# Kernel tuning notes

Hardware: AMD Instinct MI355X
Metric: run time of the kernel (lower is better)

## Reference

```python
import jax, jax.numpy as jnp
import numpy as np

ROT_DELTA = 1  # rotation_delta from __init__
BN_EPS = 1e-3  # keras BatchNormalization default epsilon


def conv_dirac(signal, bc_idx, bc_w, W, b):
    """Template-based intrinsic mesh conv (dirac patch operator).

    signal: [N, D]; bc_idx/bc_w: [N, Rr, A, 3]; W: [T, Rr, A, D]; b: [T].
    Returns [N, K, T] with K = A // ROT_DELTA rotations.
    """
    gathered = signal[bc_idx]  # [N, Rr, A, 3, D] irregular gather
    interp = jnp.einsum('vrai,vraid->vrad', bc_w, gathered)  # barycentric interp
    A = interp.shape[2]
    rots = np.arange(0, A, ROT_DELTA)
    # Rotating the (small) template weights is equivalent to rolling the
    # interpolated signal along the angular axis, but far cheaper.
    W_rot = jnp.stack([jnp.roll(W, int(r), axis=2) for r in rots])  # [K, T, Rr, A, D]
    return jnp.einsum('vrad,ktrad->vkt', interp, W_rot) + b  # [N, K, T]


def angular_max_pool(x):
    # Select, per vertex, the rotation whose response has maximal L2 norm.
    k = jnp.argmax(jnp.linalg.norm(x, axis=-1), axis=1)  # [N]
    return jnp.take_along_axis(x, k[:, None, None], axis=1)[:, 0]  # [N, T]


def batch_norm(x, gamma, beta):
    mu = jnp.mean(x, axis=0, keepdims=True)
    var = jnp.var(x, axis=0, keepdims=True)
    return gamma * (x - mu) * jax.lax.rsqrt(var + BN_EPS) + beta


def setup_inputs() -> dict:
    key = jax.random.key(0)
    ks = jax.random.split(key, 6)
    N, Rr, A, D, T = 80000, 5, 8, 32, 32
    signal = jax.random.normal(ks[0], (N, D), dtype=jnp.float32)
    bc_idx = jax.random.randint(ks[1], (N, Rr, A, 3), 0, N)
    bc_w = jax.random.uniform(ks[2], (N, Rr, A, 3), dtype=jnp.float32)
    bc_w = bc_w / jnp.sum(bc_w, axis=-1, keepdims=True)  # barycentric coords sum to 1
    W1 = jax.random.normal(ks[3], (T, Rr, A, D), dtype=jnp.float32) * 0.05
    W2 = jax.random.normal(ks[4], (T, Rr, A, D), dtype=jnp.float32) * 0.05
    return {
        'signal': signal, 'bc_idx': bc_idx, 'bc_w': bc_w,
        'W1': W1, 'b1': jnp.zeros((T,), jnp.float32),
        'gamma1': jnp.ones((T,), jnp.float32), 'beta1': jnp.zeros((T,), jnp.float32),
        'W2': W2, 'b2': jnp.zeros((T,), jnp.float32),
        'gamma2': jnp.ones((T,), jnp.float32), 'beta2': jnp.zeros((T,), jnp.float32),
    }


def reference(signal, bc_idx, bc_w, W1, b1, gamma1, beta1, W2, b2, gamma2, beta2):
    # Branch 1: conv -> angular max-pool -> BN -> relu
    s = conv_dirac(signal, bc_idx, bc_w, W1, b1)
    s = angular_max_pool(s)
    s = batch_norm(s, gamma1, beta1)
    s = jax.nn.relu(s)
    # Branch 2: conv -> angular max-pool -> BN
    s = conv_dirac(s, bc_idx, bc_w, W2, b2)
    s = angular_max_pool(s)
    s = batch_norm(s, gamma2, beta2)
    # Residual add (input_dim == amt_templates -> no rescale branch) + activation
    return jax.nn.relu(s + signal)
```

## Files before the change

### kernel.cpp

```cpp
#include <hip/hip_runtime.h>
#include <math.h>

#define RR 5
#define AA 8
#define DD 32
#define TT 32
#define KK 8
#define MM 1280

#define RT2 0.70710678118654752f

typedef float v2f __attribute__((ext_vector_type(2)));
typedef float v4f __attribute__((ext_vector_type(4)));

static __device__ __forceinline__ v2f pkfma(v2f a, v2f b, v2f c) {
#if __has_builtin(__builtin_elementwise_fma)
    return __builtin_elementwise_fma(a, b, c);
#else
    v2f r; r.x = fmaf(a.x, b.x, c.x); r.y = fmaf(a.y, b.y, c.y); return r;
#endif
}

__global__ void wdft_kernel(const float* __restrict__ W, float* __restrict__ Ws) {
    int idx = blockIdx.x * 256 + threadIdx.x;
    if (idx >= TT * RR * DD) return;
    int d = idx & 31;
    int tr = idx >> 5;
    float xa[8];
    #pragma unroll
    for (int a = 0; a < 8; ++a) xa[a] = W[(tr * 8 + a) * 32 + d];
    float s0 = xa[0] + xa[4], d0 = xa[0] - xa[4];
    float s1 = xa[1] + xa[5], d1 = xa[1] - xa[5];
    float s2 = xa[2] + xa[6], d2 = xa[2] - xa[6];
    float s3 = xa[3] + xa[7], d3 = xa[3] - xa[7];
    float s02 = s0 + s2, s13 = s1 + s3;
    float F0 = s02 + s13, F4 = s02 - s13;
    float R2 = s0 - s2, I2 = s3 - s1;
    float u = RT2 * (d1 - d3), v = RT2 * (d1 + d3);
    float R1 = d0 + u, R3 = d0 - u;
    float I1 = -d2 - v, I3 = d2 - v;
    float* o = &Ws[tr * 256 + d * 8];
    o[0] = F0; o[1] = F4; o[2] = R1; o[3] = I1;
    o[4] = R2; o[5] = I2; o[6] = R3; o[7] = I3;
}

__global__ __launch_bounds__(256, 2)
void fused_conv_kernel(const float* __restrict__ sig,
                       const int* __restrict__ bc_idx,
                       const float* __restrict__ bc_w,
                       const float* __restrict__ Wsg,
                       const float* __restrict__ bias,
                       float* __restrict__ s_out,
                       int N) {
    __shared__ float Wl[32 * 260];
    __shared__ float Is[32 * 260];

    int tid = threadIdx.x;
    int vBase = blockIdx.x * 32;

    int lane = tid & 63;
    int wv = tid >> 6;
    int vi = lane & 7;
    int tg = lane >> 3;
    int vLocal = wv * 8 + vi;
    int v = vBase + vLocal;
    bool valid = v < N;

    int d2 = tid & 15;
    int g = tid >> 4;

    v2f A0[4], A1[4], A2[4], A3[4];
    #pragma unroll
    for (int j = 0; j < 4; ++j) {
        A0[j] = (v2f){0.f, 0.f}; A1[j] = (v2f){0.f, 0.f};
        A2[j] = (v2f){0.f, 0.f}; A3[j] = (v2f){0.f, 0.f};
    }

    const float4* Ws4 = (const float4*)Wsg;
    const v2f rt2 = {RT2, RT2};

    for (int r = 0; r < RR; ++r) {
        __syncthreads();

        for (int i2 = tid; i2 < 2048; i2 += 256) {
            int t = i2 >> 6;
            int u4 = i2 & 63;
            float4 val = Ws4[(t * 5 + r) * 64 + u4];
            *(float4*)&Wl[t * 260 + u4 * 4] = val;
        }

        #pragma unroll
        for (int vv0 = 0; vv0 < 2; ++vv0) {
            int vv = g + vv0 * 16;
            int vg = vBase + vv;
            int vgc = (vg < N) ? vg : (N - 1);
            int base = (vgc * 40 + r * 8) * 3;
            v2f xa[8];
            #pragma unroll
            for (int a = 0; a < 8; ++a) {
                int i0 = bc_idx[base + a * 3 + 0];
                int i1 = bc_idx[base + a * 3 + 1];
                int i2 = bc_idx[base + a * 3 + 2];
                float w0 = bc_w[base + a * 3 + 0];
                float w1 = bc_w[base + a * 3 + 1];
                float w2 = bc_w[base + a * 3 + 2];
                v2f r0 = *(const v2f*)&sig[(size_t)i0 * 32 + 2 * d2];
                v2f r1 = *(const v2f*)&sig[(size_t)i1 * 32 + 2 * d2];
                v2f r2 = *(const v2f*)&sig[(size_t)i2 * 32 + 2 * d2];
                v2f w0v = {w0, w0};
                v2f w1v = {w1, w1};
                v2f w2v = {w2, w2};
                xa[a] = pkfma(w2v, r2, pkfma(w1v, r1, w0v * r0));
            }
            v2f s0 = xa[0] + xa[4], dd0 = xa[0] - xa[4];
            v2f s1 = xa[1] + xa[5], dd1 = xa[1] - xa[5];
            v2f s2 = xa[2] + xa[6], dd2 = xa[2] - xa[6];
            v2f s3 = xa[3] + xa[7], dd3 = xa[3] - xa[7];
            v2f s02 = s0 + s2, s13 = s1 + s3;
            v2f F0 = s02 + s13, F4 = s02 - s13;
            v2f R2 = s0 - s2, I2 = s3 - s1;
            v2f u = rt2 * (dd1 - dd3), vv_ = rt2 * (dd1 + dd3);
            v2f R1 = dd0 + u, R3 = dd0 - u;
            v2f I1 = -dd2 - vv_, I3 = dd2 - vv_;
            float* ob = &Is[vv * 260 + (2 * d2) * 8];
            v4f lo0 = {F0.x, F4.x, R1.x, I1.x};
            v4f lo1 = {R2.x, I2.x, R3.x, I3.x};
            v4f hi0 = {F0.y, F4.y, R1.y, I1.y};
            v4f hi1 = {R2.y, I2.y, R3.y, I3.y};
            *(v4f*)&ob[0] = lo0;
            *(v4f*)&ob[4] = lo1;
            *(v4f*)&ob[8] = hi0;
            *(v4f*)&ob[12] = hi1;
        }
        __syncthreads();

        const float* ip = &Is[vLocal * 260];
        const float* wp = &Wl[tg * 260];
        #pragma unroll 4
        for (int d = 0; d < 32; ++d) {
            v4f p0 = *(const v4f*)&ip[d * 8];
            v4f p1 = *(const v4f*)&ip[d * 8 + 4];
            v2f x04 = p0.xy;
            v2f x1 = p0.zw;
            v2f x2 = p1.xy;
            v2f x3 = p1.zw;
            v2f x1n = {x1.y, -x1.x};
            v2f x2n = {x2.y, -x2.x};
            v2f x3n = {x3.y, -x3.x};
            #pragma unroll
            for (int j = 0; j < 4; ++j) {
                v4f q0 = *(const v4f*)&wp[j * 8 * 260 + d * 8];
                v4f q1 = *(const v4f*)&wp[j * 8 * 260 + d * 8 + 4];
                A0[j] = pkfma(x04, q0.xy, A0[j]);
                A1[j] = pkfma(x1, (v2f){q0.z, q0.z}, A1[j]);
                A1[j] = pkfma(x1n, (v2f){q0.w, q0.w}, A1[j]);
                A2[j] = pkfma(x2, (v2f){q1.x, q1.x}, A2[j]);
                A2[j] = pkfma(x2n, (v2f){q1.y, q1.y}, A2[j]);
                A3[j] = pkfma(x3, (v2f){q1.z, q1.z}, A3[j]);
                A3[j] = pkfma(x3n, (v2f){q1.w, q1.w}, A3[j]);
            }
        }
    }

    float outk[8][4];
    #pragma unroll
    for (int j = 0; j < 4; ++j) {
        float C0 = A0[j].x, C4 = A0[j].y;
        float R1 = A1[j].x, I1 = A1[j].y;
        float R2 = A2[j].x, I2 = A2[j].y;
        float R3 = A3[j].x, I3 = A3[j].y;
        float e = 0.125f * (C0 + C4), o = 0.125f * (C0 - C4);
        float p = 0.25f * (R1 + R3), q = 0.25f * R2, s = 0.25f * (I1 - I3);
        float a_ = 0.25f * RT2 * (R1 - R3);
        float b_ = 0.25f * RT2 * (I1 + I3);
        float c_ = 0.25f * I2;
        float bb = bias[tg + 8 * j];
        outk[0][j] = e + p + q + bb;
        outk[1][j] = o + a_ - b_ - c_ + bb;
        outk[2][j] = e - s - q + bb;
        outk[3][j] = o - a_ - b_ + c_ + bb;
        outk[4][j] = e - p + q + bb;
        outk[5][j] = o - a_ + b_ - c_ + bb;
        outk[6][j] = e + s - q + bb;
        outk[7][j] = o + a_ + b_ + c_ + bb;
    }

    float best = -1.f;
    int bk = 0;
    #pragma unroll
    for (int k = 0; k < 8; ++k) {
        float nl = outk[k][0] * outk[k][0] + outk[k][1] * outk[k][1]
                 + outk[k][2] * outk[k][2] + outk[k][3] * outk[k][3];
        nl += __shfl_xor(nl, 8);
        nl += __shfl_xor(nl, 16);
        nl += __shfl_xor(nl, 32);
        float n = sqrtf(nl);
        if (n > best) { best = n; bk = k; }
    }

    if (valid) {
        float sel0 = 0.f, sel1 = 0.f, sel2 = 0.f, sel3 = 0.f;
        #pragma unroll
        for (int k = 0; k < 8; ++k) {
            if (k == bk) { sel0 = outk[k][0]; sel1 = outk[k][1]; sel2 = outk[k][2]; sel3 = outk[k][3]; }
        }
        float* o = s_out + (size_t)v * 32 + tg;
        o[0]  = sel0;
        o[8]  = sel1;
        o[16] = sel2;
        o[24] = sel3;
    }
}

__global__ void stats_kernel(const float* __restrict__ s,
                             double* __restrict__ sums,
                             double* __restrict__ sumsq, int n) {
    __shared__ double la[256];
    __shared__ double lb[256];
    int tid = threadIdx.x;
    int t = tid & 31;
    int row = tid >> 5;
    double a = 0.0, b = 0.0;
    for (int v = blockIdx.x * 8 + row; v < n; v += gridDim.x * 8) {
        float x = s[(size_t)v * 32 + t];
        a += (double)x;
        b += (double)x * (double)x;
    }
    la[tid] = a; lb[tid] = b;
    __syncthreads();
    for (int off = 128; off >= 32; off >>= 1) {
        if (tid < off) { la[tid] += la[tid + off]; lb[tid] += lb[tid + off]; }
        __syncthreads();
    }
    if (tid < 32) {
        atomicAdd(&sums[t], la[tid]);
        atomicAdd(&sumsq[t], lb[tid]);
    }
}

__global__ void finalize_kernel(const double* __restrict__ sums,
                                const double* __restrict__ sumsq,
                                const float* __restrict__ gamma,
                                const float* __restrict__ beta,
                                float* __restrict__ scale,
                                float* __restrict__ shift, int n) {
    int t = threadIdx.x;
    if (t < 32) {
        double mu = sums[t] / (double)n;
        double var = sumsq[t] / (double)n - mu * mu;
        double sc = (double)gamma[t] / sqrt(var + 1e-3);
        scale[t] = (float)sc;
        shift[t] = (float)((double)beta[t] - mu * sc);
    }
}

__global__ void affine_relu_kernel(const float* __restrict__ s,
                                   const float* __restrict__ scale,
                                   const float* __restrict__ shift,
                                   float* __restrict__ o, int n4) {
    int e = blockIdx.x * blockDim.x + threadIdx.x;
    if (e >= n4) return;
    int t0 = (e & 7) * 4;
    float4 x = ((const float4*)s)[e];
    float4 y;
    y.x = fmaxf(fmaf(scale[t0 + 0], x.x, shift[t0 + 0]), 0.f);
    y.y = fmaxf(fmaf(scale[t0 + 1], x.y, shift[t0 + 1]), 0.f);
    y.z = fmaxf(fmaf(scale[t0 + 2], x.z, shift[t0 + 2]), 0.f);
    y.w = fmaxf(fmaf(scale[t0 + 3], x.w, shift[t0 + 3]), 0.f);
    ((float4*)o)[e] = y;
}

__global__ void final_kernel(const float* __restrict__ s,
                             const float* __restrict__ scale,
                             const float* __restrict__ shift,
                             const float* __restrict__ sig,
                             float* __restrict__ o, int n4) {
    int e = blockIdx.x * blockDim.x + threadIdx.x;
    if (e >= n4) return;
    int t0 = (e & 7) * 4;
    float4 x = ((const float4*)s)[e];
    float4 z = ((const float4*)sig)[e];
    float4 y;
    y.x = fmaxf(fmaf(scale[t0 + 0], x.x, shift[t0 + 0]) + z.x, 0.f);
    y.y = fmaxf(fmaf(scale[t0 + 1], x.y, shift[t0 + 1]) + z.y, 0.f);
    y.z = fmaxf(fmaf(scale[t0 + 2], x.z, shift[t0 + 2]) + z.z, 0.f);
    y.w = fmaxf(fmaf(scale[t0 + 3], x.w, shift[t0 + 3]) + z.w, 0.f);
    ((float4*)o)[e] = y;
}

__global__ void zero_stats_kernel(double* __restrict__ d, float* __restrict__ f) {
    int t = threadIdx.x;
    if (t < 128) d[t] = 0.0;
    if (t < 128) f[t] = 0.f;
}

extern "C" void kernel_launch(void* const* d_in, const int* in_sizes, int n_in,
                              void* d_out, int out_size, void* d_ws, size_t ws_size,
                              hipStream_t stream) {
    const float* signal = (const float*)d_in[0];
    const int* bc_idx   = (const int*)d_in[1];
    const float* bc_w   = (const float*)d_in[2];
    const float* W1     = (const float*)d_in[3];
    const float* b1     = (const float*)d_in[4];
    const float* g1     = (const float*)d_in[5];
    const float* be1    = (const float*)d_in[6];
    const float* W2     = (const float*)d_in[7];
    const float* b2     = (const float*)d_in[8];
    const float* g2     = (const float*)d_in[9];
    const float* be2    = (const float*)d_in[10];
    float* out = (float*)d_out;

    const int N = in_sizes[0] / 32;

    char* ws = (char*)d_ws;
    double* sums1  = (double*)ws;
    double* sumsq1 = sums1 + 32;
    double* sums2  = sums1 + 64;
    double* sumsq2 = sums1 + 96;
    float* scale1 = (float*)(ws + 1024);
    float* shift1 = scale1 + 32;
    float* scale2 = scale1 + 64;
    float* shift2 = scale1 + 96;
    float* Ws1 = (float*)(ws + 4096);
    float* Ws2 = Ws1 + TT * RR * 256;
    float* s1  = Ws2 + TT * RR * 256;
    float* sg2 = s1 + (size_t)N * 32;
    float* s2  = sg2 + (size_t)N * 32;

    int nBlocks = (N + 31) / 32;
    int wBlocks = (TT * RR * DD + 255) / 256;

    zero_stats_kernel<<<1, 128, 0, stream>>>((double*)ws, (float*)(ws + 1024));
    wdft_kernel<<<wBlocks, 256, 0, stream>>>(W1, Ws1);
    wdft_kernel<<<wBlocks, 256, 0, stream>>>(W2, Ws2);

    fused_conv_kernel<<<nBlocks, 256, 0, stream>>>(signal, bc_idx, bc_w, Ws1, b1, s1, N);
    stats_kernel<<<64, 256, 0, stream>>>(s1, sums1, sumsq1, N);
    finalize_kernel<<<1, 32, 0, stream>>>(sums1, sumsq1, g1, be1, scale1, shift1, N);
    affine_relu_kernel<<<(N * 8 + 255) / 256, 256, 0, stream>>>(s1, scale1, shift1, sg2, N * 8);

    fused_conv_kernel<<<nBlocks, 256, 0, stream>>>(sg2, bc_idx, bc_w, Ws2, b2, s2, N);
    stats_kernel<<<64, 256, 0, stream>>>(s2, sums2, sumsq2, N);
    finalize_kernel<<<1, 32, 0, stream>>>(sums2, sumsq2, g2, be2, scale2, shift2, N);

    final_kernel<<<(N * 8 + 255) / 256, 256, 0, stream>>>(s2, scale2, shift2, signal, out, N * 8);
}
```

Measured before the change: 748.5 us.

## Restructure conv to 64 vertices per block with wave-uniform scalar weight loads

Each block now handles 64 vertices, with each lane owning one vertex and each wave owning 8 templates. The frequency-domain weights are re-laid out so a wave reads them via wave-uniform (scalar) global loads, which removes the LDS weight staging. The rotation-norm reduction across template groups now goes through a small shared buffer instead of lane shuffles, and outputs are written as vector stores. The costs are more accumulator registers (64 floats per lane), a larger shared footprint for the interpolated signal, and one more block barrier.

```diff
diff --git a/kernel.cpp b/kernel.cpp
--- a/kernel.cpp
+++ b/kernel.cpp
@@ -6,7 +6,6 @@
 #define DD 32
 #define TT 32
 #define KK 8
-#define MM 1280
 
 #define RT2 0.70710678118654752f
 
@@ -26,6 +25,8 @@
     if (idx >= TT * RR * DD) return;
     int d = idx & 31;
     int tr = idx >> 5;
+    int t = tr / 5;
+    int r = tr - t * 5;
     float xa[8];
     #pragma unroll
     for (int a = 0; a < 8; ++a) xa[a] = W[(tr * 8 + a) * 32 + d];
@@ -39,7 +40,7 @@
     float u = RT2 * (d1 - d3), v = RT2 * (d1 + d3);
     float R1 = d0 + u, R3 = d0 - u;
     float I1 = -d2 - v, I3 = d2 - v;
-    float* o = &Ws[tr * 256 + d * 8];
+    float* o = &Ws[(size_t)(((r * 4 + (t >> 3)) * 32 + d) * 64) + (t & 7) * 8];
     o[0] = F0; o[1] = F4; o[2] = R1; o[3] = I1;
     o[4] = R2; o[5] = I2; o[6] = R3; o[7] = I3;
 }
@@ -52,45 +53,32 @@
                        const float* __restrict__ bias,
                        float* __restrict__ s_out,
                        int N) {
-    __shared__ float Wl[32 * 260];
-    __shared__ float Is[32 * 260];
+    __shared__ float Is[64 * 260];
+    __shared__ float red[64 * 36];
 
     int tid = threadIdx.x;
-    int vBase = blockIdx.x * 32;
-
+    int vBase = blockIdx.x * 64;
     int lane = tid & 63;
     int wv = tid >> 6;
-    int vi = lane & 7;
-    int tg = lane >> 3;
-    int vLocal = wv * 8 + vi;
-    int v = vBase + vLocal;
+    int v = vBase + lane;
     bool valid = v < N;
 
     int d2 = tid & 15;
     int g = tid >> 4;
 
-    v2f A0[4], A1[4], A2[4], A3[4];
-    #pragma unroll
-    for (int j = 0; j < 4; ++j) {
-        A0[j] = (v2f){0.f, 0.f}; A1[j] = (v2f){0.f, 0.f};
-        A2[j] = (v2f){0.f, 0.f}; A3[j] = (v2f){0.f, 0.f};
-    }
-
-    const float4* Ws4 = (const float4*)Wsg;
+    float acc[8][8];
+    #pragma unroll
+    for (int ti = 0; ti < 8; ++ti)
+        #pragma unroll
+        for (int f = 0; f < 8; ++f) acc[ti][f] = 0.f;
+
     const v2f rt2 = {RT2, RT2};
 
     for (int r = 0; r < RR; ++r) {
         __syncthreads();
 
-        for (int i2 = tid; i2 < 2048; i2 += 256) {
-            int t = i2 >> 6;
-            int u4 = i2 & 63;
-            float4 val = Ws4[(t * 5 + r) * 64 + u4];
-            *(float4*)&Wl[t * 260 + u4 * 4] = val;
-        }
-
-        #pragma unroll
-        for (int vv0 = 0; vv0 < 2; ++vv0) {
+        #pragma unroll
+        for (int vv0 = 0; vv0 < 4; ++vv0) {
             int vv = g + vv0 * 16;
             int vg = vBase + vv;
             int vgc = (vg < N) ? vg : (N - 1);
@@ -134,81 +122,106 @@
         }
         __syncthreads();
 
-        const float* ip = &Is[vLocal * 260];
-        const float* wp = &Wl[tg * 260];
-        #pragma unroll 4
+        const float* ip = &Is[lane * 260];
+        int woff = __builtin_amdgcn_readfirstlane((r * 4 + wv) * 2048);
+        const float* wr = Wsg + woff;
+        #pragma unroll 2
         for (int d = 0; d < 32; ++d) {
             v4f p0 = *(const v4f*)&ip[d * 8];
             v4f p1 = *(const v4f*)&ip[d * 8 + 4];
-            v2f x04 = p0.xy;
-            v2f x1 = p0.zw;
-            v2f x2 = p1.xy;
-            v2f x3 = p1.zw;
-            v2f x1n = {x1.y, -x1.x};
-            v2f x2n = {x2.y, -x2.x};
-            v2f x3n = {x3.y, -x3.x};
+            const float* wd = wr + d * 64;
             #pragma unroll
-            for (int j = 0; j < 4; ++j) {
-                v4f q0 = *(const v4f*)&wp[j * 8 * 260 + d * 8];
-                v4f q1 = *(const v4f*)&wp[j * 8 * 260 + d * 8 + 4];
-                A0[j] = pkfma(x04, q0.xy, A0[j]);
-                A1[j] = pkfma(x1, (v2f){q0.z, q0.z}, A1[j]);
-                A1[j] = pkfma(x1n, (v2f){q0.w, q0.w}, A1[j]);
-                A2[j] = pkfma(x2, (v2f){q1.x, q1.x}, A2[j]);
-                A2[j] = pkfma(x2n, (v2f){q1.y, q1.y}, A2[j]);
-                A3[j] = pkfma(x3, (v2f){q1.z, q1.z}, A3[j]);
-                A3[j] = pkfma(x3n, (v2f){q1.w, q1.w}, A3[j]);
+            for (int ti = 0; ti < 8; ++ti) {
+                float w0 = wd[ti * 8 + 0];
+                float w1 = wd[ti * 8 + 1];
+                float w2 = wd[ti * 8 + 2];
+                float w3 = wd[ti * 8 + 3];
+                float w4 = wd[ti * 8 + 4];
+                float w5 = wd[ti * 8 + 5];
+                float w6 = wd[ti * 8 + 6];
+                float w7 = wd[ti * 8 + 7];
+                acc[ti][0] = fmaf(p0.x, w0, acc[ti][0]);
+                acc[ti][1] = fmaf(p0.y, w1, acc[ti][1]);
+                acc[ti][2] = fmaf(p0.z, w2, fmaf(p0.w, w3, acc[ti][2]));
+                acc[ti][3] = fmaf(p0.w, w2, fmaf(-p0.z, w3, acc[ti][3]));
+                acc[ti][4] = fmaf(p1.x, w4, fmaf(p1.y, w5, acc[ti][4]));
+                acc[ti][5] = fmaf(p1.y, w4, fmaf(-p1.x, w5, acc[ti][5]));
+                acc[ti][6] = fmaf(p1.z, w6, fmaf(p1.w, w7, acc[ti][6]));
+                acc[ti][7] = fmaf(p1.w, w6, fmaf(-p1.z, w7, acc[ti][7]));
             }
         }
     }
 
-    float outk[8][4];
-    #pragma unroll
-    for (int j = 0; j < 4; ++j) {
-        float C0 = A0[j].x, C4 = A0[j].y;
-        float R1 = A1[j].x, I1 = A1[j].y;
-        float R2 = A2[j].x, I2 = A2[j].y;
-        float R3 = A3[j].x, I3 = A3[j].y;
+    float outk[8][8];
+    #pragma unroll
+    for (int ti = 0; ti < 8; ++ti) {
+        float C0 = acc[ti][0], C4 = acc[ti][1];
+        float R1 = acc[ti][2], I1 = acc[ti][3];
+        float R2 = acc[ti][4], I2 = acc[ti][5];
+        float R3 = acc[ti][6], I3 = acc[ti][7];
         float e = 0.125f * (C0 + C4), o = 0.125f * (C0 - C4);
         float p = 0.25f * (R1 + R3), q = 0.25f * R2, s = 0.25f * (I1 - I3);
         float a_ = 0.25f * RT2 * (R1 - R3);
         float b_ = 0.25f * RT2 * (I1 + I3);
         float c_ = 0.25f * I2;
-        float bb = bias[tg + 8 * j];
-        outk[0][j] = e + p + q + bb;
-        outk[1][j] = o + a_ - b_ - c_ + bb;
-        outk[2][j] = e - s - q + bb;
-        outk[3][j] = o - a_ - b_ + c_ + bb;
-        outk[4][j] = e - p + q + bb;
-        outk[5][j] = o - a_ + b_ - c_ + bb;
-        outk[6][j] = e + s - q + bb;
-        outk[7][j] = o + a_ + b_ + c_ + bb;
-    }
-
+        float bb = bias[wv * 8 + ti];
+        outk[0][ti] = e + p + q + bb;
+        outk[1][ti] = o + a_ - b_ - c_ + bb;
+        outk[2][ti] = e - s - q + bb;
+        outk[3][ti] = o - a_ - b_ + c_ + bb;
+        outk[4][ti] = e - p + q + bb;
+        outk[5][ti] = o - a_ + b_ - c_ + bb;
+        outk[6][ti] = e + s - q + bb;
+        outk[7][ti] = o + a_ + b_ + c_ + bb;
+    }
+
+    float pn[8];
+    #pragma unroll
+    for (int k = 0; k < 8; ++k) {
+        float s = 0.f;
+        #pragma unroll
+        for (int ti = 0; ti < 8; ++ti) s = fmaf(outk[k][ti], outk[k][ti], s);
+        pn[k] = s;
+    }
+    {
+        float* rb = &red[lane * 36 + wv * 8];
+        *(v4f*)&rb[0] = (v4f){pn[0], pn[1], pn[2], pn[3]};
+        *(v4f*)&rb[4] = (v4f){pn[4], pn[5], pn[6], pn[7]};
+    }
+    __syncthreads();
+
+    float norms[8];
+    #pragma unroll
+    for (int k = 0; k < 8; ++k) norms[k] = 0.f;
+    #pragma unroll
+    for (int w = 0; w < 4; ++w) {
+        v4f a = *(const v4f*)&red[lane * 36 + w * 8];
+        v4f b = *(const v4f*)&red[lane * 36 + w * 8 + 4];
+        norms[0] += a.x; norms[1] += a.y; norms[2] += a.z; norms[3] += a.w;
+        norms[4] += b.x; norms[5] += b.y; norms[6] += b.z; norms[7] += b.w;
+    }
     float best = -1.f;
     int bk = 0;
     #pragma unroll
     for (int k = 0; k < 8; ++k) {
-        float nl = outk[k][0] * outk[k][0] + outk[k][1] * outk[k][1]
-                 + outk[k][2] * outk[k][2] + outk[k][3] * outk[k][3];
-        nl += __shfl_xor(nl, 8);
-        nl += __shfl_xor(nl, 16);
-        nl += __shfl_xor(nl, 32);
-        float n = sqrtf(nl);
+        float n = sqrtf(norms[k]);
         if (n > best) { best = n; bk = k; }
     }
 
     if (valid) {
-        float sel0 = 0.f, sel1 = 0.f, sel2 = 0.f, sel3 = 0.f;
+        float sel[8];
+        #pragma unroll
+        for (int ti = 0; ti < 8; ++ti) sel[ti] = 0.f;
         #pragma unroll
         for (int k = 0; k < 8; ++k) {
-            if (k == bk) { sel0 = outk[k][0]; sel1 = outk[k][1]; sel2 = outk[k][2]; sel3 = outk[k][3]; }
+            if (k == bk) {
+                #pragma unroll
+                for (int ti = 0; ti < 8; ++ti) sel[ti] = outk[k][ti];
+            }
         }
-        float* o = s_out + (size_t)v * 32 + tg;
-        o[0]  = sel0;
-        o[8]  = sel1;
-        o[16] = sel2;
-        o[24] = sel3;
+        float* o = s_out + (size_t)v * 32 + wv * 8;
+        *(v4f*)&o[0] = (v4f){sel[0], sel[1], sel[2], sel[3]};
+        *(v4f*)&o[4] = (v4f){sel[4], sel[5], sel[6], sel[7]};
     }
 }
 
@@ -327,7 +340,7 @@
     float* sg2 = s1 + (size_t)N * 32;
     float* s2  = sg2 + (size_t)N * 32;
 
-    int nBlocks = (N + 31) / 32;
+    int nBlocks = (N + 63) / 64;
     int wBlocks = (TT * RR * DD + 255) / 256;
 
     zero_stats_kernel<<<1, 128, 0, stream>>>((double*)ws, (float*)(ws + 1024));
```

After: 1.433 ms. 1.91x slower.
